# Kernel optimization log

Measured on AMD Instinct MI355X. Metric: run time of the kernel, lower is better.

## Reference

```python
import jax, jax.numpy as jnp
import numpy as np

VOXEL_SIZE = 0.4
STRIDE = 2
NUM_BATCH = 4
PRE_MAXSIZE = 1024  # nms_premaxsize
NMS_THR = 0.1
NEG_INF = -1e9


def setup_inputs() -> dict:
    key = jax.random.key(0)
    ks = jax.random.split(key, 7)
    N, C = 200000, 256
    feat = jax.random.normal(ks[0], (N, C), dtype=jnp.float32)
    batch_idx = jax.random.randint(ks[1], (N,), 0, NUM_BATCH, dtype=jnp.int32)
    coor = jax.random.randint(ks[2], (N, 2), 0, 400, dtype=jnp.int32)
    W_cls = jax.random.normal(ks[3], (C, 2), dtype=jnp.float32) * 0.02
    b_cls = jnp.zeros((2,), dtype=jnp.float32)
    W_reg = jax.random.normal(ks[4], (C, 9), dtype=jnp.float32) * 0.02
    b_reg = jnp.zeros((9,), dtype=jnp.float32)
    return {"feat": feat, "batch_idx": batch_idx, "coor": coor,
            "W_cls": W_cls, "b_cls": b_cls, "W_reg": W_reg, "b_reg": b_reg}


def _bev_iou(bx):
    # bx: [K,7] (x,y,z,l,w,h,r); axis-aligned BEV IoU on (x,y,l,w)
    x, y, l, w = bx[:, 0], bx[:, 1], bx[:, 3], bx[:, 4]
    x1, x2 = x - l / 2, x + l / 2
    y1, y2 = y - w / 2, y + w / 2
    ix = jnp.maximum(jnp.minimum(x2[:, None], x2[None, :]) - jnp.maximum(x1[:, None], x1[None, :]), 0.0)
    iy = jnp.maximum(jnp.minimum(y2[:, None], y2[None, :]) - jnp.maximum(y1[:, None], y1[None, :]), 0.0)
    inter = ix * iy
    area = l * w
    union = area[:, None] + area[None, :] - inter
    return inter / jnp.maximum(union, 1e-6)


def _nms_keep(iou):
    # greedy NMS over score-descending rows; returns keep mask [K]
    K = iou.shape[0]
    idx = jnp.arange(K)

    def body(i, supp):
        keep_i = jnp.logical_not(supp[i])
        new = keep_i & (iou[i] > NMS_THR) & (idx > i)
        return supp | new

    supp = jax.lax.fori_loop(0, K, body, jnp.zeros((K,), dtype=bool))
    return jnp.logical_not(supp)


def reference(feat, batch_idx, coor, W_cls, b_cls, W_reg, b_reg):
    # ---- shared heads over all sparse voxels ----
    cls_logits = feat @ W_cls + b_cls            # [N, 1+1] (neg evidence, class)
    probs = jax.nn.softmax(cls_logits, axis=-1)
    cls_prob = probs[:, 1:]                      # [N, n_cls]
    conf = jnp.max(cls_prob, axis=-1)            # [N]
    label = jnp.argmax(cls_prob, axis=-1)        # [N]

    reg = feat @ W_reg + b_reg                   # [N, 9] -> ctr(3) dim(3) dir(2) scr(1)
    ctr, dim, drn, scr = reg[:, :3], reg[:, 3:6], reg[:, 6:8], reg[:, 8]
    scr = jax.nn.sigmoid(scr)                    # sigmoid_keys=['scr']

    # indices2metric: voxel indices -> metric centers
    centers = coor.astype(jnp.float32) * (VOXEL_SIZE * STRIDE)  # [N, 2]

    xy = centers + ctr[:, :2]
    z = ctr[:, 2]
    lwh = jnp.exp(jnp.clip(dim, -6.0, 6.0))
    angle = jnp.arctan2(drn[:, 0], drn[:, 1])
    boxes = jnp.concatenate([xy, z[:, None], lwh, angle[:, None]], axis=-1)  # [N, 7]
    score = conf * scr                           # [N]

    def per_sample(b):
        s = jnp.where(batch_idx == b, score, NEG_INF)
        vals, idx = jax.lax.top_k(s, PRE_MAXSIZE)          # score-sorted (desc)
        bx = boxes[idx]                                     # [K, 7]
        lb = label[idx]                                     # [K]
        valid = vals > NEG_INF / 2
        iou = _bev_iou(bx)
        keep = _nms_keep(iou) & valid
        out = jnp.concatenate([bx, vals[:, None]], axis=-1) * keep[:, None]  # [K, 8]
        return out, lb, keep

    out, lb, keep = jax.vmap(per_sample)(jnp.arange(NUM_BATCH))
    return out, lb, keep
```

## Files before the change

### kernel.cpp

```cpp
#include <hip/hip_runtime.h>
#include <math.h>

#define NBATCH 4
#define PRE 1024
#define CAND 4096
#define NHIST 65536
#define MAXSLOT 384

__device__ __forceinline__ unsigned long long allow_mask(int i, int l) {
    int base = l << 6;
    if (i < base) return ~0ull;
    int sh = i - base + 1;
    if (sh >= 64) return 0ull;
    return (~0ull) << sh;
}

__global__ void k0_weights(const float* __restrict__ Wcls, const float* __restrict__ bcls,
                           const float* __restrict__ Wreg, const float* __restrict__ breg,
                           double* __restrict__ Wd3, float* __restrict__ Wf8,
                           double* __restrict__ biasD, float* __restrict__ biasF) {
    int j = blockIdx.x;
    int c = threadIdx.x;
    if (j < 2) {
        Wd3[j * 256 + c] = (double)Wcls[c * 2 + j];
        if (c == 0) biasD[j] = (double)bcls[j];
    } else if (j == 10) {
        Wd3[2 * 256 + c] = (double)Wreg[c * 9 + 8];
        if (c == 0) biasD[2] = (double)breg[8];
    } else {
        int r = j - 2;
        Wf8[r * 256 + c] = Wreg[c * 9 + r];
        if (c == 0) biasF[r] = breg[r];
    }
}

__global__ __launch_bounds__(256) void k1_points(
    const float4* __restrict__ feat4, const int* __restrict__ batch_idx,
    const int* __restrict__ coor, const double* __restrict__ Wd3,
    const float* __restrict__ Wf8, const double* __restrict__ biasD,
    const float* __restrict__ biasF, float* __restrict__ pointData,
    unsigned long long* __restrict__ keys, unsigned int* __restrict__ hist, int N) {
    __shared__ float4 smem4[64 * 68 / 4];
    float* sfeat = (float*)smem4;
    int tid = threadIdx.x;
    int q = tid >> 6;
    int p = tid & 63;
    int p0 = blockIdx.x * 64;

    double accD0 = 0.0, accD1 = 0.0, accD2 = 0.0;
    float accF[8];
#pragma unroll
    for (int j = 0; j < 8; ++j) accF[j] = 0.f;

    for (int c = 0; c < 4; ++c) {
        __syncthreads();
#pragma unroll
        for (int it = 0; it < 4; ++it) {
            int u = it * 256 + tid;
            int pl = u >> 4, f4 = u & 15;
            int gp = p0 + pl;
            float4 v = make_float4(0.f, 0.f, 0.f, 0.f);
            if (gp < N) v = feat4[(size_t)gp * 64 + c * 16 + f4];
            *(float4*)(sfeat + pl * 68 + f4 * 4) = v;
        }
        __syncthreads();
        int chb = c * 64 + q * 16;
        const double* w0 = Wd3 + chb;
        const float* wf = Wf8 + chb;
#pragma unroll
        for (int k4 = 0; k4 < 4; ++k4) {
            float4 v = *(const float4*)(sfeat + p * 68 + q * 16 + k4 * 4);
            float vv[4] = {v.x, v.y, v.z, v.w};
#pragma unroll
            for (int m = 0; m < 4; ++m) {
                int k = k4 * 4 + m;
                double fd = (double)vv[m];
                accD0 = fma(fd, w0[k], accD0);
                accD1 = fma(fd, w0[256 + k], accD1);
                accD2 = fma(fd, w0[512 + k], accD2);
#pragma unroll
                for (int j = 0; j < 8; ++j) accF[j] = fmaf(vv[m], wf[j * 256 + k], accF[j]);
            }
        }
    }
    __syncthreads();
    double* pD = (double*)smem4;
    float* pF = (float*)smem4 + 1536;
    pD[tid * 3 + 0] = accD0; pD[tid * 3 + 1] = accD1; pD[tid * 3 + 2] = accD2;
#pragma unroll
    for (int j = 0; j < 8; ++j) pF[tid * 8 + j] = accF[j];
    __syncthreads();
    if (tid < 64) {
        int gp = p0 + tid;
        if (gp < N) {
            double d0 = biasD[0], d1 = biasD[1], d2 = biasD[2];
            float f[8];
#pragma unroll
            for (int j = 0; j < 8; ++j) f[j] = biasF[j];
#pragma unroll
            for (int qq = 0; qq < 4; ++qq) {
                int base = qq * 64 + tid;
                d0 += pD[base * 3 + 0]; d1 += pD[base * 3 + 1]; d2 += pD[base * 3 + 2];
#pragma unroll
                for (int j = 0; j < 8; ++j) f[j] += pF[base * 8 + j];
            }
            double conf = 1.0 / (1.0 + exp(-(d1 - d0)));
            double scr = 1.0 / (1.0 + exp(-d2));
            double score = conf * scr;
            float s32 = (float)score;

            float cx = (float)coor[2 * gp] * 0.8f;
            float cy = (float)coor[2 * gp + 1] * 0.8f;
            float bx = cx + f[0], by = cy + f[1], bz = f[2];
            float bl = expf(fminf(fmaxf(f[3], -6.f), 6.f));
            float bw = expf(fminf(fmaxf(f[4], -6.f), 6.f));
            float bh = expf(fminf(fmaxf(f[5], -6.f), 6.f));
            float ba = atan2f(f[6], f[7]);

            float4* pd = (float4*)(pointData + (size_t)gp * 8);
            pd[0] = make_float4(bx, by, bz, bl);
            pd[1] = make_float4(bw, bh, ba, s32);
            keys[gp] = (unsigned long long)__double_as_longlong(score);
            int b = batch_idx[gp];
            atomicAdd(&hist[b * NHIST + (__float_as_uint(s32) >> 16)], 1u);
        }
    }
}

__global__ __launch_bounds__(256) void k2_thresh(const unsigned int* __restrict__ hist,
                                                 unsigned int* __restrict__ Tarr) {
    int b = blockIdx.x, tid = threadIdx.x;
    __shared__ unsigned int csum[256];
    __shared__ unsigned int chunkv[256];
    __shared__ int stc;
    __shared__ unsigned int scum;
    const unsigned int* h = hist + b * NHIST;
    unsigned int s = 0;
    for (int m = 0; m < 256; ++m) s += h[tid * 256 + m];
    csum[tid] = s;
    __syncthreads();
    if (tid == 0) {
        unsigned int cum = 0; int tc = -1;
        for (int t = 255; t >= 0; --t) {
            if (cum + csum[t] >= 1024u) { tc = t; break; }
            cum += csum[t];
        }
        stc = tc; scum = cum;
    }
    __syncthreads();
    int tc = stc;
    if (tc < 0) { if (tid == 0) Tarr[b] = 0u; return; }
    chunkv[tid] = h[tc * 256 + tid];
    __syncthreads();
    if (tid == 0) {
        unsigned int cum = scum, T = (unsigned int)(tc * 256);
        for (int m = 255; m >= 0; --m) {
            unsigned int c = chunkv[m];
            if (cum + c >= 1024u) { T = (unsigned int)(tc * 256 + m); break; }
            cum += c;
        }
        Tarr[b] = T;
    }
}

__global__ void k3_compact(const int* __restrict__ batch_idx, const float* __restrict__ pointData,
                           const unsigned long long* __restrict__ keys,
                           const unsigned int* __restrict__ Tarr, unsigned int* __restrict__ candCount,
                           unsigned int* __restrict__ candIdx, unsigned long long* __restrict__ candKey,
                           int N) {
    int p = blockIdx.x * 256 + threadIdx.x;
    if (p >= N) return;
    int b = batch_idx[p];
    float s32 = pointData[(size_t)p * 8 + 7];
    unsigned int bucket = __float_as_uint(s32) >> 16;
    if (bucket >= Tarr[b]) {
        unsigned int pos = atomicAdd(&candCount[b], 1u);
        if (pos < CAND) {
            candIdx[b * CAND + pos] = (unsigned int)p;
            candKey[b * CAND + pos] = keys[p];
        }
    }
}

__global__ __launch_bounds__(1024) void k4_sort(const unsigned int* __restrict__ candCount,
                                                const unsigned int* __restrict__ candIdx,
                                                const unsigned long long* __restrict__ candKey,
                                                const float* __restrict__ pointData,
                                                float* __restrict__ topBox,
                                                unsigned int* __restrict__ validArr) {
    int b = blockIdx.x, tid = threadIdx.x;
    __shared__ unsigned long long ka[CAND];
    __shared__ unsigned int id[CAND];
    unsigned int cnt = candCount[b];
    if (cnt > CAND) cnt = CAND;
    int n = (cnt <= 2048u) ? 2048 : 4096;
    for (int t = tid; t < n; t += 1024) {
        if ((unsigned int)t < cnt) {
            ka[t] = ~candKey[b * CAND + t];
            id[t] = candIdx[b * CAND + t];
        } else {
            ka[t] = ~0ull;
            id[t] = 0xFFFFFFFFu;
        }
    }
    __syncthreads();
    for (int k = 2; k <= n; k <<= 1) {
        for (int j = k >> 1; j > 0; j >>= 1) {
            for (int t = tid; t < n; t += 1024) {
                int l = t ^ j;
                if (l > t) {
                    bool up = ((t & k) == 0);
                    unsigned long long kt = ka[t], kl = ka[l];
                    unsigned int it_ = id[t], il = id[l];
                    bool gt = (kt > kl) || (kt == kl && it_ > il);
                    if (gt == up) { ka[t] = kl; ka[l] = kt; id[t] = il; id[l] = it_; }
                }
            }
            __syncthreads();
        }
    }
    unsigned int gi = id[tid];
    bool valid = (gi != 0xFFFFFFFFu) && ((unsigned int)tid < cnt);
    float v[8];
#pragma unroll
    for (int k = 0; k < 8; ++k) v[k] = 0.f;
    if (valid) {
        const float* pd = pointData + (size_t)gi * 8;
#pragma unroll
        for (int k = 0; k < 8; ++k) v[k] = pd[k];
    }
    float* tb = topBox + (size_t)(b * PRE + tid) * 8;
#pragma unroll
    for (int k = 0; k < 8; ++k) tb[k] = v[k];
    validArr[b * PRE + tid] = valid ? 1u : 0u;
}

__global__ __launch_bounds__(256) void k5_iou(const float* __restrict__ topBox,
                                              unsigned long long* __restrict__ M) {
    int wid = blockIdx.x * 4 + (threadIdx.x >> 6);
    int lane = threadIdx.x & 63;
    int b = wid >> 14;
    int rem = wid & 16383;
    int i = rem >> 4;
    int wj = rem & 15;
    if (wj < (i >> 6)) return;
    const float* bi = topBox + (size_t)(b * PRE + i) * 8;
    int j = wj * 64 + lane;
    const float* bj = topBox + (size_t)(b * PRE + j) * 8;
    float xi = bi[0], yi = bi[1], li = bi[3], wi_ = bi[4];
    float xj = bj[0], yj = bj[1], lj = bj[3], wj_ = bj[4];
    float x1i = xi - li * 0.5f, x2i = xi + li * 0.5f;
    float y1i = yi - wi_ * 0.5f, y2i = yi + wi_ * 0.5f;
    float x1j = xj - lj * 0.5f, x2j = xj + lj * 0.5f;
    float y1j = yj - wj_ * 0.5f, y2j = yj + wj_ * 0.5f;
    float ix = fmaxf(fminf(x2i, x2j) - fmaxf(x1i, x1j), 0.0f);
    float iy = fmaxf(fminf(y2i, y2j) - fmaxf(y1i, y1j), 0.0f);
    float inter = ix * iy;
    float ai = li * wi_, aj = lj * wj_;
    float uni = ai + aj - inter;
    float iou = inter / fmaxf(uni, 1e-6f);
    unsigned long long m = __ballot(iou > 0.1f);
    if (lane == 0) M[(size_t)(b * PRE + i) * 16 + wj] = m;
}

__global__ __launch_bounds__(256) void k6_nms(const unsigned long long* __restrict__ M,
                                              const unsigned int* __restrict__ validArr,
                                              const float* __restrict__ topBox,
                                              float* __restrict__ out0,
                                              float* __restrict__ keepOut) {
    __shared__ unsigned long long Mc[MAXSLOT * 16];
    __shared__ unsigned int slotIdx[PRE];
    __shared__ unsigned int cntSh;
    __shared__ unsigned long long suppSh[16];
    int b = blockIdx.x, tid = threadIdx.x;
    if (tid == 0) cntSh = 0;
    __syncthreads();
    for (int r = tid; r < PRE; r += 256) {
        const unsigned long long* row = M + (size_t)(b * PRE + r) * 16;
        unsigned long long w[16];
        unsigned long long o = 0ull;
#pragma unroll
        for (int l = 0; l < 16; ++l) { w[l] = row[l] & allow_mask(r, l); o |= w[l]; }
        unsigned int s = 0xFFFFFFFFu;
        if (o != 0ull) {
            unsigned int slot = atomicAdd(&cntSh, 1u);
            if (slot < MAXSLOT) {
                s = slot;
#pragma unroll
                for (int l = 0; l < 16; ++l) Mc[slot * 16 + l] = w[l];
            } else s = 0xFFFFFFFEu;
        }
        slotIdx[r] = s;
    }
    __syncthreads();
    if (tid < 64) {
        int lane = tid;
        unsigned long long supp = 0ull;
        for (int g = 0; g < 16; ++g) {
            unsigned long long act = __ballot(slotIdx[g * 64 + lane] != 0xFFFFFFFFu);
            while (act) {
                int bit = __builtin_ctzll(act);
                act &= act - 1ull;
                int i = g * 64 + bit;
                unsigned long long wsup = __shfl(supp, g);
                bool keep_i = ((wsup >> (i & 63)) & 1ull) == 0ull;
                if (keep_i && lane < 16) {
                    unsigned int s = slotIdx[i];
                    unsigned long long add = (s < MAXSLOT)
                        ? Mc[s * 16 + lane]
                        : (M[(size_t)(b * PRE + i) * 16 + lane] & allow_mask(i, lane));
                    supp |= add;
                }
            }
        }
        if (lane < 16) suppSh[lane] = supp;
    }
    __syncthreads();
    for (int r = tid; r < PRE; r += 256) {
        bool keep = (((suppSh[r >> 6] >> (r & 63)) & 1ull) == 0ull) && (validArr[b * PRE + r] != 0u);
        float kf = keep ? 1.0f : 0.0f;
        const float* tb = topBox + (size_t)(b * PRE + r) * 8;
        float* o = out0 + (size_t)(b * PRE + r) * 8;
#pragma unroll
        for (int k = 0; k < 8; ++k) o[k] = tb[k] * kf;
        keepOut[b * PRE + r] = kf;
    }
}

extern "C" void kernel_launch(void* const* d_in, const int* in_sizes, int n_in,
                              void* d_out, int out_size, void* d_ws, size_t ws_size,
                              hipStream_t stream) {
    int N = in_sizes[0] / 256;
    const float* feat = (const float*)d_in[0];
    const int* batch_idx = (const int*)d_in[1];
    const int* coor = (const int*)d_in[2];
    const float* Wcls = (const float*)d_in[3];
    const float* bcls = (const float*)d_in[4];
    const float* Wreg = (const float*)d_in[5];
    const float* breg = (const float*)d_in[6];

    char* ws = (char*)d_ws;
    size_t off = 0;
    auto take = [&](size_t bytes) -> char* {
        char* r = ws + off;
        off += (bytes + 255) & ~(size_t)255;
        return r;
    };
    float* pointData = (float*)take((size_t)N * 8 * 4);
    unsigned long long* keys = (unsigned long long*)take((size_t)N * 8);
    unsigned int* hist = (unsigned int*)take((size_t)NBATCH * NHIST * 4);
    unsigned int* Tarr = (unsigned int*)take(NBATCH * 4);
    unsigned int* candCount = (unsigned int*)take(NBATCH * 4);
    unsigned int* candIdx = (unsigned int*)take(NBATCH * CAND * 4);
    unsigned long long* candKey = (unsigned long long*)take(NBATCH * CAND * 8);
    float* topBox = (float*)take(NBATCH * PRE * 8 * 4);
    unsigned int* validArr = (unsigned int*)take(NBATCH * PRE * 4);
    unsigned long long* M = (unsigned long long*)take((size_t)NBATCH * PRE * 16 * 8);
    double* Wd3 = (double*)take(3 * 256 * 8);
    float* Wf8 = (float*)take(8 * 256 * 4);
    double* biasD = (double*)take(3 * 8);
    float* biasF = (float*)take(8 * 4);

    float* out0 = (float*)d_out;
    float* keepOut = out0 + NBATCH * PRE * 8 + NBATCH * PRE;

    hipMemsetAsync(d_out, 0, (size_t)out_size * 4, stream);
    hipMemsetAsync(hist, 0, (size_t)NBATCH * NHIST * 4, stream);
    hipMemsetAsync(candCount, 0, NBATCH * 4, stream);

    int pb64 = (N + 63) / 64;
    int pb256 = (N + 255) / 256;
    k0_weights<<<dim3(11), dim3(256), 0, stream>>>(Wcls, bcls, Wreg, breg, Wd3, Wf8, biasD, biasF);
    k1_points<<<dim3(pb64), dim3(256), 0, stream>>>((const float4*)feat, batch_idx, coor,
                                                    Wd3, Wf8, biasD, biasF,
                                                    pointData, keys, hist, N);
    k2_thresh<<<dim3(NBATCH), dim3(256), 0, stream>>>(hist, Tarr);
    k3_compact<<<dim3(pb256), dim3(256), 0, stream>>>(batch_idx, pointData, keys, Tarr,
                                                      candCount, candIdx, candKey, N);
    k4_sort<<<dim3(NBATCH), dim3(1024), 0, stream>>>(candCount, candIdx, candKey,
                                                     pointData, topBox, validArr);
    k5_iou<<<dim3(NBATCH * PRE * 16 / 4), dim3(256), 0, stream>>>(topBox, M);
    k6_nms<<<dim3(NBATCH), dim3(256), 0, stream>>>(M, validArr, topBox, out0, keepOut);
}
```

Measured before the change: 488.4 us.

## Restructure point head kernel with async global-to-LDS double buffering

The point head kernel now assigns one point per thread (256 points per block) instead of splitting channels across four waves, which removes the cross-wave partial-sum reduction through shared memory. Feature rows are streamed in 32-channel chunks straight into LDS with global_load_lds, using an XOR swizzle to avoid bank conflicts, and double buffered so the next chunk loads while the current one is computed. The cost is 64 KB of LDS per block, which lowers occupancy. Each thread also reads all 256 weight channels per point, and out-of-range rows are clamped to the last point.

```diff
diff --git a/kernel.cpp b/kernel.cpp
--- a/kernel.cpp
+++ b/kernel.cpp
@@ -6,6 +6,13 @@
 #define CAND 4096
 #define NHIST 65536
 #define MAXSLOT 384
+
+typedef __attribute__((address_space(1))) const void GlbVoid;
+typedef __attribute__((address_space(3))) void LdsVoid;
+
+__device__ __forceinline__ void gld_lds16(const void* g, void* l) {
+    __builtin_amdgcn_global_load_lds((GlbVoid*)g, (LdsVoid*)l, 16, 0, 0);
+}
 
 __device__ __forceinline__ unsigned long long allow_mask(int i, int l) {
     int base = l << 6;
@@ -35,95 +42,89 @@
 }
 
 __global__ __launch_bounds__(256) void k1_points(
-    const float4* __restrict__ feat4, const int* __restrict__ batch_idx,
+    const float* __restrict__ feat, const int* __restrict__ batch_idx,
     const int* __restrict__ coor, const double* __restrict__ Wd3,
     const float* __restrict__ Wf8, const double* __restrict__ biasD,
     const float* __restrict__ biasF, float* __restrict__ pointData,
     unsigned long long* __restrict__ keys, unsigned int* __restrict__ hist, int N) {
-    __shared__ float4 smem4[64 * 68 / 4];
-    float* sfeat = (float*)smem4;
-    int tid = threadIdx.x;
-    int q = tid >> 6;
-    int p = tid & 63;
-    int p0 = blockIdx.x * 64;
+    __shared__ float sbuf[2][256 * 32];
+    const int tid = threadIdx.x;
+    const int w = tid >> 6, lane = tid & 63;
+    const int p0 = blockIdx.x * 256;
 
     double accD0 = 0.0, accD1 = 0.0, accD2 = 0.0;
     float accF[8];
 #pragma unroll
     for (int j = 0; j < 8; ++j) accF[j] = 0.f;
 
-    for (int c = 0; c < 4; ++c) {
+    const int s_src = (lane & 7) ^ (lane >> 3);
+
+    auto stage = [&](int buf, int ch) {
+#pragma unroll
+        for (int it = 0; it < 8; ++it) {
+            int R0 = w * 64 + it * 8;
+            int r = R0 + (lane >> 3);
+            int gp = p0 + r;
+            if (gp >= N) gp = N - 1;
+            const float* g = feat + (size_t)gp * 256 + ch * 32 + s_src * 4;
+            gld_lds16(g, &sbuf[buf][R0 * 32]);
+        }
+    };
+
+    auto compute = [&](int buf, int ch) {
+        const float* row = &sbuf[buf][tid * 32];
+        const int rs = tid & 7;
+#pragma unroll
+        for (int k4 = 0; k4 < 8; ++k4) {
+            const float4 v = *(const float4*)(row + ((k4 ^ rs) * 4));
+            const int cb = ch * 32 + k4 * 4;
+            float vv[4] = {v.x, v.y, v.z, v.w};
+#pragma unroll
+            for (int m = 0; m < 4; ++m) {
+                int c = cb + m;
+                double fd = (double)vv[m];
+                accD0 = fma(fd, Wd3[c], accD0);
+                accD1 = fma(fd, Wd3[256 + c], accD1);
+                accD2 = fma(fd, Wd3[512 + c], accD2);
+#pragma unroll
+                for (int j = 0; j < 8; ++j) accF[j] = fmaf(vv[m], Wf8[j * 256 + c], accF[j]);
+            }
+        }
+    };
+
+    stage(0, 0);
+    __syncthreads();
+    for (int ch = 0; ch < 8; ++ch) {
+        if (ch < 7) stage((ch + 1) & 1, ch + 1);
+        compute(ch & 1, ch);
         __syncthreads();
-#pragma unroll
-        for (int it = 0; it < 4; ++it) {
-            int u = it * 256 + tid;
-            int pl = u >> 4, f4 = u & 15;
-            int gp = p0 + pl;
-            float4 v = make_float4(0.f, 0.f, 0.f, 0.f);
-            if (gp < N) v = feat4[(size_t)gp * 64 + c * 16 + f4];
-            *(float4*)(sfeat + pl * 68 + f4 * 4) = v;
-        }
-        __syncthreads();
-        int chb = c * 64 + q * 16;
-        const double* w0 = Wd3 + chb;
-        const float* wf = Wf8 + chb;
-#pragma unroll
-        for (int k4 = 0; k4 < 4; ++k4) {
-            float4 v = *(const float4*)(sfeat + p * 68 + q * 16 + k4 * 4);
-            float vv[4] = {v.x, v.y, v.z, v.w};
-#pragma unroll
-            for (int m = 0; m < 4; ++m) {
-                int k = k4 * 4 + m;
-                double fd = (double)vv[m];
-                accD0 = fma(fd, w0[k], accD0);
-                accD1 = fma(fd, w0[256 + k], accD1);
-                accD2 = fma(fd, w0[512 + k], accD2);
-#pragma unroll
-                for (int j = 0; j < 8; ++j) accF[j] = fmaf(vv[m], wf[j * 256 + k], accF[j]);
-            }
-        }
-    }
-    __syncthreads();
-    double* pD = (double*)smem4;
-    float* pF = (float*)smem4 + 1536;
-    pD[tid * 3 + 0] = accD0; pD[tid * 3 + 1] = accD1; pD[tid * 3 + 2] = accD2;
-#pragma unroll
-    for (int j = 0; j < 8; ++j) pF[tid * 8 + j] = accF[j];
-    __syncthreads();
-    if (tid < 64) {
-        int gp = p0 + tid;
-        if (gp < N) {
-            double d0 = biasD[0], d1 = biasD[1], d2 = biasD[2];
-            float f[8];
-#pragma unroll
-            for (int j = 0; j < 8; ++j) f[j] = biasF[j];
-#pragma unroll
-            for (int qq = 0; qq < 4; ++qq) {
-                int base = qq * 64 + tid;
-                d0 += pD[base * 3 + 0]; d1 += pD[base * 3 + 1]; d2 += pD[base * 3 + 2];
-#pragma unroll
-                for (int j = 0; j < 8; ++j) f[j] += pF[base * 8 + j];
-            }
-            double conf = 1.0 / (1.0 + exp(-(d1 - d0)));
-            double scr = 1.0 / (1.0 + exp(-d2));
-            double score = conf * scr;
-            float s32 = (float)score;
-
-            float cx = (float)coor[2 * gp] * 0.8f;
-            float cy = (float)coor[2 * gp + 1] * 0.8f;
-            float bx = cx + f[0], by = cy + f[1], bz = f[2];
-            float bl = expf(fminf(fmaxf(f[3], -6.f), 6.f));
-            float bw = expf(fminf(fmaxf(f[4], -6.f), 6.f));
-            float bh = expf(fminf(fmaxf(f[5], -6.f), 6.f));
-            float ba = atan2f(f[6], f[7]);
-
-            float4* pd = (float4*)(pointData + (size_t)gp * 8);
-            pd[0] = make_float4(bx, by, bz, bl);
-            pd[1] = make_float4(bw, bh, ba, s32);
-            keys[gp] = (unsigned long long)__double_as_longlong(score);
-            int b = batch_idx[gp];
-            atomicAdd(&hist[b * NHIST + (__float_as_uint(s32) >> 16)], 1u);
-        }
+    }
+
+    int gp = p0 + tid;
+    if (gp < N) {
+        double d0 = biasD[0] + accD0, d1 = biasD[1] + accD1, d2 = biasD[2] + accD2;
+        float f[8];
+#pragma unroll
+        for (int j = 0; j < 8; ++j) f[j] = biasF[j] + accF[j];
+        double conf = 1.0 / (1.0 + exp(-(d1 - d0)));
+        double scr = 1.0 / (1.0 + exp(-d2));
+        double score = conf * scr;
+        float s32 = (float)score;
+
+        float cx = (float)coor[2 * gp] * 0.8f;
+        float cy = (float)coor[2 * gp + 1] * 0.8f;
+        float bx = cx + f[0], by = cy + f[1], bz = f[2];
+        float bl = expf(fminf(fmaxf(f[3], -6.f), 6.f));
+        float bw = expf(fminf(fmaxf(f[4], -6.f), 6.f));
+        float bh = expf(fminf(fmaxf(f[5], -6.f), 6.f));
+        float ba = atan2f(f[6], f[7]);
+
+        float4* pd = (float4*)(pointData + (size_t)gp * 8);
+        pd[0] = make_float4(bx, by, bz, bl);
+        pd[1] = make_float4(bw, bh, ba, s32);
+        keys[gp] = (unsigned long long)__double_as_longlong(score);
+        int b = batch_idx[gp];
+        atomicAdd(&hist[b * NHIST + (__float_as_uint(s32) >> 16)], 1u);
     }
 }
 
@@ -368,14 +369,13 @@
     hipMemsetAsync(hist, 0, (size_t)NBATCH * NHIST * 4, stream);
     hipMemsetAsync(candCount, 0, NBATCH * 4, stream);
 
-    int pb64 = (N + 63) / 64;
-    int pb256 = (N + 255) / 256;
+    int pbPts = (N + 255) / 256;
     k0_weights<<<dim3(11), dim3(256), 0, stream>>>(Wcls, bcls, Wreg, breg, Wd3, Wf8, biasD, biasF);
-    k1_points<<<dim3(pb64), dim3(256), 0, stream>>>((const float4*)feat, batch_idx, coor,
-                                                    Wd3, Wf8, biasD, biasF,
-                                                    pointData, keys, hist, N);
+    k1_points<<<dim3(pbPts), dim3(256), 0, stream>>>(feat, batch_idx, coor,
+                                                     Wd3, Wf8, biasD, biasF,
+                                                     pointData, keys, hist, N);
     k2_thresh<<<dim3(NBATCH), dim3(256), 0, stream>>>(hist, Tarr);
-    k3_compact<<<dim3(pb256), dim3(256), 0, stream>>>(batch_idx, pointData, keys, Tarr,
+    k3_compact<<<dim3(pbPts), dim3(256), 0, stream>>>(batch_idx, pointData, keys, Tarr,
                                                       candCount, candIdx, candKey, N);
     k4_sort<<<dim3(NBATCH), dim3(1024), 0, stream>>>(candCount, candIdx, candKey,
                                                      pointData, topBox, validArr);
```

Measured after the change: 470.0 us. -3.8%, faster.
